# Optimization experiments

Hardware: AMD Instinct MI355X
Metric: run time of the kernel (lower is better)

The kernel has to match this reference:

```python
import jax, jax.numpy as jnp
import numpy as np

B, S, E = 8, 2048, 512
H = 8
LN_EPS = 1e-5


def _layer_norm(x, g, b):
    mu = jnp.mean(x, axis=-1, keepdims=True)
    var = jnp.mean((x - mu) ** 2, axis=-1, keepdims=True)
    return (x - mu) * jax.lax.rsqrt(var + LN_EPS) * g + b


def setup_inputs() -> dict:
    key = jax.random.key(0)
    ks = jax.random.split(key, 16)
    sc = 1.0 / np.sqrt(E)
    return {
        "q": jax.random.normal(ks[0], (B, S, E), jnp.float32),
        "k": jax.random.normal(ks[1], (B, S, E), jnp.float32),
        "trajectories": jax.random.normal(ks[2], (B, S, E), jnp.float32),
        "v_W": jax.random.normal(ks[3], (E, E), jnp.float32) * sc,
        "v_b": jnp.zeros((E,), jnp.float32),
        "out_W": jax.random.normal(ks[4], (E, E), jnp.float32) * sc,
        "out_b": jnp.zeros((E,), jnp.float32),
        "ln1_g": jnp.ones((E,), jnp.float32),
        "ln1_b": jnp.zeros((E,), jnp.float32),
        "ffn_w1": jax.random.normal(ks[5], (E, E), jnp.float32) * sc,
        "ffn_b1": jnp.zeros((E,), jnp.float32),
        "ffn_w2": jax.random.normal(ks[6], (E, E), jnp.float32) * sc,
        "ffn_b2": jnp.zeros((E,), jnp.float32),
        "ln2_g": jnp.ones((E,), jnp.float32),
        "ln2_b": jnp.zeros((E,), jnp.float32),
    }


def reference(q, k, trajectories, v_W, v_b, out_W, out_b, ln1_g, ln1_b,
              ffn_w1, ffn_b1, ffn_w2, ffn_b2, ln2_g, ln2_b):
    seq_len = q.shape[1]
    # V projection (v = k in the block's call). q_linear/k_linear are unused in the original forward.
    V = k @ v_W + v_b  # [B,S,E]; head split + per-head matmul + concat == single matmul

    # Multi-view trajectory similarity (TSMiniSimilarity), averaged over 4 views
    tn = trajectories / jnp.maximum(
        jnp.linalg.norm(trajectories, axis=-1, keepdims=True), 1e-12)
    c = jnp.einsum('bie,bje->bij', tn, tn)  # cosine similarity [B,S,S]
    aw = (jax.nn.sigmoid(c)
          + jax.nn.sigmoid(c * c)
          + jax.nn.sigmoid(jnp.exp(c - 1.0))
          + jax.nn.sigmoid(0.5 * c + 0.5)) * 0.25

    # First softmax over keys
    aw = jax.nn.softmax(aw, axis=-1)
    # ut_mask = triu(ones, diag=1); original fills where mask == 0 (lower triangle incl. diag)
    ut = jnp.triu(jnp.ones((seq_len, seq_len), dtype=bool), k=1)
    aw = jnp.where(ut, aw, -1e9)
    # Second softmax after masking
    aw = jax.nn.softmax(aw, axis=-1)

    attended = jnp.einsum('bij,bje->bie', aw, V)
    attn_out = attended @ out_W + out_b

    x = _layer_norm(q + attn_out, ln1_g, ln1_b)  # dropout is identity in eval
    h = jax.nn.relu(x @ ffn_w1 + ffn_b1) @ ffn_w2 + ffn_b2
    return _layer_norm(x + h, ln2_g, ln2_b)
```

## Files before the change

### kernel.cpp

```cpp
#include <hip/hip_runtime.h>

typedef __attribute__((ext_vector_type(8))) short s8v;
typedef __attribute__((ext_vector_type(4))) short s4v;
typedef __attribute__((ext_vector_type(4))) float f4v;

constexpr int SEQ = 2048;
constexpr int EMB = 512;
constexpr int BATCH = 8;
constexpr int BS = BATCH * SEQ;
constexpr int NCH = 32;

#define DEVINL __device__ __forceinline__

DEVINL float bf2f(short s) {
    union { unsigned u; float f; } v;
    v.u = ((unsigned)(unsigned short)s) << 16;
    return v.f;
}
DEVINL short f2bf(float f) {
    union { float f; unsigned u; } v; v.f = f;
    unsigned u = v.u;
    return (short)((u + 0x7FFFu + ((u >> 16) & 1u)) >> 16);
}
DEVINL f4v mfma16(s8v a, s8v b, f4v c) {
    return __builtin_amdgcn_mfma_f32_16x16x32_bf16(a, b, c, 0, 0, 0);
}
DEVINL s8v pack8(float4 a, float4 b) {
    s8v o;
    o[0] = f2bf(a.x); o[1] = f2bf(a.y); o[2] = f2bf(a.z); o[3] = f2bf(a.w);
    o[4] = f2bf(b.x); o[5] = f2bf(b.y); o[6] = f2bf(b.z); o[7] = f2bf(b.w);
    return o;
}
DEVINL void gload16(const short* g, short* l) {
    __builtin_amdgcn_global_load_lds(
        (const __attribute__((address_space(1))) void*)g,
        (__attribute__((address_space(3))) void*)l, 16, 0, 0);
}

__global__ __launch_bounds__(256) void prep_combo(
    const float* __restrict__ v_W, const float* __restrict__ out_W,
    const float* __restrict__ w1, const float* __restrict__ w2,
    const float* __restrict__ K, const float* __restrict__ v_b,
    const float* __restrict__ out_b,
    short* __restrict__ VWb, short* __restrict__ WoT,
    short* __restrict__ W1T, short* __restrict__ W2T,
    float* __restrict__ partial, float* __restrict__ bc) {
    __shared__ __attribute__((aligned(16))) char smem[4 * EMB * 4];
    const int blk = blockIdx.x;
    const int tid = threadIdx.x;

    if (blk < 128) {
        int i = blk * 256 + tid;
        const float* p = v_W + (size_t)i * 8;
        float4 a = *(const float4*)p;
        float4 b = *(const float4*)(p + 4);
        *(s8v*)(VWb + (size_t)i * 8) = pack8(a, b);
    } else if (blk < 320) {
        __shared__ short tile[64][72];
        int t = blk - 128;
        int sel = t >> 6;
        const float* W = (sel == 0) ? out_W : (sel == 1 ? w1 : w2);
        short* WT = (sel == 0) ? WoT : (sel == 1 ? W1T : W2T);
        int tileid = t & 63;
        int kt = (tileid >> 3) * 64, nt = (tileid & 7) * 64;
        int r = tid >> 4;
        int c4 = (tid & 15) * 4;
#pragma unroll
        for (int p = 0; p < 4; p++) {
            int row = p * 16 + r;
            float4 v = *(const float4*)(W + (size_t)(kt + row) * EMB + nt + c4);
            tile[row][c4 + 0] = f2bf(v.x);
            tile[row][c4 + 1] = f2bf(v.y);
            tile[row][c4 + 2] = f2bf(v.z);
            tile[row][c4 + 3] = f2bf(v.w);
        }
        __syncthreads();
        int kl = (tid & 7) * 8;
        int nl = tid >> 3;
#pragma unroll
        for (int h = 0; h < 2; h++) {
            int n = h * 32 + nl;
            s8v o;
#pragma unroll
            for (int e = 0; e < 8; e++) o[e] = tile[kl + e][n];
            *(s8v*)(WT + (size_t)(nt + n) * EMB + kt + kl) = o;
        }
    } else if (blk < 576) {
        float* sh = (float*)smem;
        int bb = blk - 320;
        int b = bb >> 5, c = bb & (NCH - 1);
        int g = tid >> 6, lane = tid & 63;
        int col8 = lane * 8;
        const float* base = K + ((size_t)b * SEQ + c * 64 + g * 16) * EMB + col8;
        float acc[8] = {};
        for (int it = 0; it < 16; it++) {
            float4 a = *(const float4*)(base + (size_t)it * EMB);
            float4 b2 = *(const float4*)(base + (size_t)it * EMB + 4);
            acc[0] += a.x; acc[1] += a.y; acc[2] += a.z; acc[3] += a.w;
            acc[4] += b2.x; acc[5] += b2.y; acc[6] += b2.z; acc[7] += b2.w;
        }
#pragma unroll
        for (int j = 0; j < 8; j++) sh[g * EMB + col8 + j] = acc[j];
        __syncthreads();
        if (g == 0) {
#pragma unroll
            for (int j = 0; j < 8; j++) {
                int e = col8 + j;
                partial[((size_t)b * NCH + c) * EMB + e] =
                    sh[e] + sh[EMB + e] + sh[2 * EMB + e] + sh[3 * EMB + e];
            }
        }
    } else {
        float* sh = (float*)smem;
        int bb = blk - 576;
        int nl = tid & 31, ms = tid >> 5;
        int n = bb * 32 + nl;
        float acc = 0.f;
#pragma unroll 8
        for (int mm = 0; mm < 64; mm++) {
            int m = ms * 64 + mm;
            acc = fmaf(v_b[m], out_W[(size_t)m * EMB + n], acc);
        }
        sh[tid] = acc;
        __syncthreads();
        if (tid < 32) {
            float s = 0.f;
#pragma unroll
            for (int j = 0; j < 8; j++) s += sh[j * 32 + tid];
            bc[bb * 32 + tid] = s + out_b[bb * 32 + tid];
        }
    }
}

template <int EPI>
__global__ __launch_bounds__(256, 2) void mgemm(
    const short* __restrict__ A, const short* __restrict__ B,
    const float* __restrict__ bias, short* __restrict__ C) {
    __shared__ __attribute__((aligned(16))) short lds[2][16384];

    const int nwg = gridDim.x;
    const int q = nwg >> 3;
    const int bid = blockIdx.x;
    const int wg = (bid & 7) * q + (bid >> 3);
    const int mt = wg >> 2, nt = wg & 3;
    const int mbase = mt * 128, nbase = nt * 128;

    const int tid = threadIdx.x;
    const int w = tid >> 6, lane = tid & 63;
    const int lr = lane & 15, kg = lane >> 4;
    const int wr = w >> 1, wc = w & 1;

    const short* gA[4];
    const short* gB[4];
    short* lA[4];
    short* lB[4];
#pragma unroll
    for (int inst = 0; inst < 4; inst++) {
        int U = inst * 256 + w * 64 + lane;
        int row = U >> 3, cu = U & 7;
        int csrc = cu ^ (row & 7);
        gA[inst] = A + (size_t)(mbase + row) * EMB + csrc * 8;
        gB[inst] = B + (size_t)(nbase + row) * EMB + csrc * 8;
        lA[inst] = &lds[0][(inst * 256 + w * 64) * 8];
        lB[inst] = &lds[0][8192 + (inst * 256 + w * 64) * 8];
    }

    int aoff[4][2], boff[4][2];
#pragma unroll
    for (int m = 0; m < 4; m++)
#pragma unroll
        for (int ks = 0; ks < 2; ks++) {
            int row = wr * 64 + m * 16 + lr;
            int cu = (ks * 4 + kg) ^ (row & 7);
            aoff[m][ks] = row * 64 + cu * 8;
        }
#pragma unroll
    for (int n = 0; n < 4; n++)
#pragma unroll
        for (int ks = 0; ks < 2; ks++) {
            int row = wc * 64 + n * 16 + lr;
            int cu = (ks * 4 + kg) ^ (row & 7);
            boff[n][ks] = 8192 + row * 64 + cu * 8;
        }

    auto stage = [&](int kt, int d) {
        int koff = kt * 64;
        int dd = d * 16384;
#pragma unroll
        for (int inst = 0; inst < 4; inst++)
            gload16(gA[inst] + koff, lA[inst] + dd);
#pragma unroll
        for (int inst = 0; inst < 4; inst++)
            gload16(gB[inst] + koff, lB[inst] + dd);
    };

    f4v acc[4][4] = {};
    stage(0, 0);
    int cur = 0;
    for (int kt = 0; kt < 8; kt++) {
        __syncthreads();
        if (kt < 7) stage(kt + 1, cur ^ 1);
        const short* base = &lds[cur][0];
        s8v afr[4][2], bfr[4][2];
#pragma unroll
        for (int m = 0; m < 4; m++)
#pragma unroll
            for (int ks = 0; ks < 2; ks++)
                afr[m][ks] = *(const s8v*)(base + aoff[m][ks]);
#pragma unroll
        for (int n = 0; n < 4; n++)
#pragma unroll
            for (int ks = 0; ks < 2; ks++)
                bfr[n][ks] = *(const s8v*)(base + boff[n][ks]);
#pragma unroll
        for (int ks = 0; ks < 2; ks++)
#pragma unroll
            for (int m = 0; m < 4; m++)
#pragma unroll
                for (int n = 0; n < 4; n++)
                    acc[m][n] = mfma16(afr[m][ks], bfr[n][ks], acc[m][n]);
        cur ^= 1;
    }

    if constexpr (EPI == 2) {
#pragma unroll
        for (int m = 0; m < 4; m++)
#pragma unroll
            for (int n = 0; n < 4; n++) {
                int col = nbase + wc * 64 + n * 16 + lr;
                int row0 = mbase + wr * 64 + m * 16 + kg * 4;
                s4v o;
#pragma unroll
                for (int r = 0; r < 4; r++) o[r] = f2bf(acc[m][n][r]);
                *(s4v*)(C + (size_t)col * EMB + row0) = o;
            }
    } else {
        float bcol[4];
#pragma unroll
        for (int n = 0; n < 4; n++)
            bcol[n] = bias[nbase + wc * 64 + n * 16 + lr];
#pragma unroll
        for (int m = 0; m < 4; m++)
#pragma unroll
            for (int n = 0; n < 4; n++) {
                int col = nbase + wc * 64 + n * 16 + lr;
#pragma unroll
                for (int r = 0; r < 4; r++) {
                    int row = mbase + wr * 64 + m * 16 + kg * 4 + r;
                    float v = acc[m][n][r] + bcol[n];
                    if constexpr (EPI == 1) v = fmaxf(v, 0.f);
                    C[(size_t)row * EMB + col] = f2bf(v);
                }
            }
    }
}

__global__ __launch_bounds__(256) void scan_p2(const float* __restrict__ K,
                                               const float* __restrict__ partial,
                                               short* __restrict__ SK) {
    __shared__ float wsum[4][EMB];
    int b = blockIdx.x >> 5, c = blockIdx.x & (NCH - 1);
    int g = threadIdx.x >> 6, lane = threadIdx.x & 63;
    int col8 = lane * 8;

    float off[8] = {}, alltot[8] = {};
    for (int cc = 0; cc < NCH; cc++) {
        const float* pp = partial + ((size_t)b * NCH + cc) * EMB + col8;
        float4 pa = *(const float4*)pp;
        float4 pb = *(const float4*)(pp + 4);
        float v[8] = {pa.x, pa.y, pa.z, pa.w, pb.x, pb.y, pb.z, pb.w};
#pragma unroll
        for (int j = 0; j < 8; j++) {
            alltot[j] += v[j];
            if (cc > c) off[j] += v[j];
        }
    }
    const float* base = K + ((size_t)b * SEQ + c * 64 + g * 16) * EMB + col8;
    {
        float acc[8] = {};
        for (int it = 0; it < 16; it++) {
            float4 a = *(const float4*)(base + (size_t)it * EMB);
            float4 bb = *(const float4*)(base + (size_t)it * EMB + 4);
            acc[0] += a.x; acc[1] += a.y; acc[2] += a.z; acc[3] += a.w;
            acc[4] += bb.x; acc[5] += bb.y; acc[6] += bb.z; acc[7] += bb.w;
        }
#pragma unroll
        for (int j = 0; j < 8; j++) wsum[g][col8 + j] = acc[j];
    }
    __syncthreads();
    float suf[8];
#pragma unroll
    for (int j = 0; j < 8; j++) {
        float s = off[j];
        for (int gg = g + 1; gg < 4; gg++) s += wsum[gg][col8 + j];
        suf[j] = s;
    }
    short* skbase = SK + ((size_t)b * SEQ + c * 64 + g * 16) * EMB + col8;
    for (int it = 15; it >= 0; it--) {
        int gi = c * 64 + g * 16 + it;
        float4 a = *(const float4*)(base + (size_t)it * EMB);
        float4 bb = *(const float4*)(base + (size_t)it * EMB + 4);
        s8v o;
        if (gi == SEQ - 1) {
            float inv = 1.0f / (float)SEQ;
#pragma unroll
            for (int j = 0; j < 8; j++) o[j] = f2bf(alltot[j] * inv);
        } else {
            float inv = __builtin_amdgcn_rcpf((float)(SEQ - 1 - gi));
#pragma unroll
            for (int j = 0; j < 8; j++) o[j] = f2bf(suf[j] * inv);
        }
        *(s8v*)(skbase + (size_t)it * EMB) = o;
        suf[0] += a.x; suf[1] += a.y; suf[2] += a.z; suf[3] += a.w;
        suf[4] += bb.x; suf[5] += bb.y; suf[6] += bb.z; suf[7] += bb.w;
    }
}

__global__ __launch_bounds__(256) void ln1_kernel(
    const float* __restrict__ q, const short* __restrict__ VO2,
    const float* __restrict__ gam, const float* __restrict__ bet,
    short* __restrict__ Xbf) {
    int w = threadIdx.x >> 6, lane = threadIdx.x & 63;
    int row0 = blockIdx.x * 32 + w * 8;
    for (int it = 0; it < 8; it++) {
        size_t grow = row0 + it;
        const float* qp = q + grow * EMB + lane * 8;
        float4 qa = *(const float4*)qp;
        float4 qb = *(const float4*)(qp + 4);
        s8v ao = *(const s8v*)(VO2 + grow * EMB + lane * 8);
        float v[8];
        v[0] = qa.x + bf2f(ao[0]); v[1] = qa.y + bf2f(ao[1]);
        v[2] = qa.z + bf2f(ao[2]); v[3] = qa.w + bf2f(ao[3]);
        v[4] = qb.x + bf2f(ao[4]); v[5] = qb.y + bf2f(ao[5]);
        v[6] = qb.z + bf2f(ao[6]); v[7] = qb.w + bf2f(ao[7]);
        float s = 0.f, t = 0.f;
#pragma unroll
        for (int j = 0; j < 8; j++) { s += v[j]; t += v[j] * v[j]; }
#pragma unroll
        for (int m = 32; m >= 1; m >>= 1) {
            s += __shfl_xor(s, m);
            t += __shfl_xor(t, m);
        }
        float mean = s * (1.f / EMB);
        float var = t * (1.f / EMB) - mean * mean;
        float rstd = rsqrtf(var + 1e-5f);
        s8v xb;
#pragma unroll
        for (int j = 0; j < 8; j++) {
            int col = lane * 8 + j;
            xb[j] = f2bf((v[j] - mean) * rstd * gam[col] + bet[col]);
        }
        *(s8v*)(Xbf + grow * EMB + lane * 8) = xb;
    }
}

__global__ __launch_bounds__(256) void ln2_kernel(
    const short* __restrict__ Xbf, const short* __restrict__ Y,
    const float* __restrict__ gam, const float* __restrict__ bet,
    float* __restrict__ out) {
    int w = threadIdx.x >> 6, lane = threadIdx.x & 63;
    int row0 = blockIdx.x * 32 + w * 8;
    for (int it = 0; it < 8; it++) {
        size_t grow = row0 + it;
        s8v xv = *(const s8v*)(Xbf + grow * EMB + lane * 8);
        s8v yv = *(const s8v*)(Y + grow * EMB + lane * 8);
        float v[8];
#pragma unroll
        for (int j = 0; j < 8; j++) v[j] = bf2f(xv[j]) + bf2f(yv[j]);
        float s = 0.f, t = 0.f;
#pragma unroll
        for (int j = 0; j < 8; j++) { s += v[j]; t += v[j] * v[j]; }
#pragma unroll
        for (int m = 32; m >= 1; m >>= 1) {
            s += __shfl_xor(s, m);
            t += __shfl_xor(t, m);
        }
        float mean = s * (1.f / EMB);
        float var = t * (1.f / EMB) - mean * mean;
        float rstd = rsqrtf(var + 1e-5f);
        float xo[8];
#pragma unroll
        for (int j = 0; j < 8; j++) {
            int col = lane * 8 + j;
            xo[j] = (v[j] - mean) * rstd * gam[col] + bet[col];
        }
        float* op = out + grow * EMB + lane * 8;
        *(float4*)op = make_float4(xo[0], xo[1], xo[2], xo[3]);
        *(float4*)(op + 4) = make_float4(xo[4], xo[5], xo[6], xo[7]);
    }
}


extern "C" void kernel_launch(void* const* d_in, const int* in_sizes, int n_in,
                              void* d_out, int out_size, void* d_ws, size_t ws_size,
                              hipStream_t stream) {
    (void)in_sizes; (void)n_in; (void)out_size; (void)ws_size;
    const float* q     = (const float*)d_in[0];
    const float* k     = (const float*)d_in[1];
    const float* v_W   = (const float*)d_in[3];
    const float* v_b   = (const float*)d_in[4];
    const float* out_W = (const float*)d_in[5];
    const float* out_b = (const float*)d_in[6];
    const float* ln1_g = (const float*)d_in[7];
    const float* ln1_b = (const float*)d_in[8];
    const float* w1    = (const float*)d_in[9];
    const float* b1    = (const float*)d_in[10];
    const float* w2    = (const float*)d_in[11];
    const float* b2    = (const float*)d_in[12];
    const float* ln2_g = (const float*)d_in[13];
    const float* ln2_b = (const float*)d_in[14];

    char* ws = (char*)d_ws;
    const size_t MB = 1u << 20;
    short* SK   = (short*)(ws);
    short* VO2  = (short*)(ws + 16 * MB);
    short* Xbf  = (short*)(ws + 32 * MB);
    short* H1   = (short*)(ws + 48 * MB);
    short* Y    = (short*)(ws + 64 * MB);
    short* VWb  = (short*)(ws + 80 * MB);
    short* WoT  = VWb + 512 * 512;
    short* W1T  = WoT + 512 * 512;
    short* W2T  = W1T + 512 * 512;
    short* WcT  = W2T + 512 * 512;
    float* bc   = (float*)(WcT + 512 * 512);
    float* part = bc + EMB;

    prep_combo<<<592, 256, 0, stream>>>(v_W, out_W, w1, w2, k, v_b, out_b,
                                        VWb, WoT, W1T, W2T, part, bc);
    mgemm<2><<<(EMB / 128) * 4, 256, 0, stream>>>(VWb, WoT, nullptr, WcT);
    scan_p2<<<BATCH * NCH, 256, 0, stream>>>(k, part, SK);
    mgemm<0><<<(BS / 128) * 4, 256, 0, stream>>>(SK, WcT, bc, VO2);
    ln1_kernel<<<BS / 32, 256, 0, stream>>>(q, VO2, ln1_g, ln1_b, Xbf);
    mgemm<1><<<(BS / 128) * 4, 256, 0, stream>>>(Xbf, W1T, b1, H1);
    mgemm<0><<<(BS / 128) * 4, 256, 0, stream>>>(H1, W2T, b2, Y);
    ln2_kernel<<<BS / 32, 256, 0, stream>>>(Xbf, Y, ln2_g, ln2_b, (float*)d_out);
}
```

Measured before the change: 104.3 us.

## Fuse all stages into one persistent kernel with grid-wide barriers

Replaces eight separate kernel launches with one persistent kernel of 512 blocks that runs every stage (weight prep, scan, four GEMMs, two layernorms) and separates them with a software grid barrier built on atomics. The aim is to remove launch overhead and the idle tails between dependent kernels. It relies on all 512 blocks being co-resident (two per CU with 64KB LDS each), otherwise the barrier deadlocks. Each barrier is a serialising point with atomic spinning, and the shared 64KB LDS buffer may lower occupancy for the non-GEMM phases.

```diff
diff --git a/kernel.cpp b/kernel.cpp
--- a/kernel.cpp
+++ b/kernel.cpp
@@ -9,6 +9,7 @@
 constexpr int BATCH = 8;
 constexpr int BS = BATCH * SEQ;
 constexpr int NCH = 32;
+constexpr int NBLK = 512;
 
 #define DEVINL __device__ __forceinline__
 
@@ -37,27 +38,42 @@
         (__attribute__((address_space(3))) void*)l, 16, 0, 0);
 }
 
-__global__ __launch_bounds__(256) void prep_combo(
-    const float* __restrict__ v_W, const float* __restrict__ out_W,
-    const float* __restrict__ w1, const float* __restrict__ w2,
-    const float* __restrict__ K, const float* __restrict__ v_b,
-    const float* __restrict__ out_b,
-    short* __restrict__ VWb, short* __restrict__ WoT,
-    short* __restrict__ W1T, short* __restrict__ W2T,
-    float* __restrict__ partial, float* __restrict__ bc) {
-    __shared__ __attribute__((aligned(16))) char smem[4 * EMB * 4];
-    const int blk = blockIdx.x;
-    const int tid = threadIdx.x;
-
-    if (blk < 128) {
-        int i = blk * 256 + tid;
+DEVINL void gridbar(unsigned* cnt, unsigned* gen) {
+    __syncthreads();
+    if (threadIdx.x == 0) {
+        unsigned g = __hip_atomic_load(gen, __ATOMIC_RELAXED,
+                                       __HIP_MEMORY_SCOPE_AGENT);
+        unsigned a = __hip_atomic_fetch_add(cnt, 1u, __ATOMIC_ACQ_REL,
+                                            __HIP_MEMORY_SCOPE_AGENT);
+        if (a == (unsigned)(NBLK - 1)) {
+            __hip_atomic_store(cnt, 0u, __ATOMIC_RELAXED,
+                               __HIP_MEMORY_SCOPE_AGENT);
+            __hip_atomic_store(gen, g + 1u, __ATOMIC_RELEASE,
+                               __HIP_MEMORY_SCOPE_AGENT);
+        } else {
+            while (__hip_atomic_load(gen, __ATOMIC_ACQUIRE,
+                                     __HIP_MEMORY_SCOPE_AGENT) == g)
+                __builtin_amdgcn_s_sleep(2);
+        }
+    }
+    __syncthreads();
+}
+
+
+DEVINL void prep_item(int item, int tid, char* Ub,
+                      const float* v_W, const float* out_W, const float* w1,
+                      const float* w2, const float* K, const float* v_b,
+                      const float* out_b, short* VWb, short* WoT, short* W1T,
+                      short* W2T, float* partial, float* bc) {
+    if (item < 128) {
+        int i = item * 256 + tid;
         const float* p = v_W + (size_t)i * 8;
         float4 a = *(const float4*)p;
         float4 b = *(const float4*)(p + 4);
         *(s8v*)(VWb + (size_t)i * 8) = pack8(a, b);
-    } else if (blk < 320) {
-        __shared__ short tile[64][72];
-        int t = blk - 128;
+    } else if (item < 320) {
+        short(*tile)[72] = (short(*)[72])Ub;
+        int t = item - 128;
         int sel = t >> 6;
         const float* W = (sel == 0) ? out_W : (sel == 1 ? w1 : w2);
         short* WT = (sel == 0) ? WoT : (sel == 1 ? W1T : W2T);
@@ -85,9 +101,9 @@
             for (int e = 0; e < 8; e++) o[e] = tile[kl + e][n];
             *(s8v*)(WT + (size_t)(nt + n) * EMB + kt + kl) = o;
         }
-    } else if (blk < 576) {
-        float* sh = (float*)smem;
-        int bb = blk - 320;
+    } else if (item < 576) {
+        float* sh = (float*)Ub;
+        int bb = item - 320;
         int b = bb >> 5, c = bb & (NCH - 1);
         int g = tid >> 6, lane = tid & 63;
         int col8 = lane * 8;
@@ -111,8 +127,8 @@
             }
         }
     } else {
-        float* sh = (float*)smem;
-        int bb = blk - 576;
+        float* sh = (float*)Ub;
+        int bb = item - 576;
         int nl = tid & 31, ms = tid >> 5;
         int n = bb * 32 + nl;
         float acc = 0.f;
@@ -132,135 +148,11 @@
     }
 }
 
-template <int EPI>
-__global__ __launch_bounds__(256, 2) void mgemm(
-    const short* __restrict__ A, const short* __restrict__ B,
-    const float* __restrict__ bias, short* __restrict__ C) {
-    __shared__ __attribute__((aligned(16))) short lds[2][16384];
-
-    const int nwg = gridDim.x;
-    const int q = nwg >> 3;
-    const int bid = blockIdx.x;
-    const int wg = (bid & 7) * q + (bid >> 3);
-    const int mt = wg >> 2, nt = wg & 3;
-    const int mbase = mt * 128, nbase = nt * 128;
-
-    const int tid = threadIdx.x;
-    const int w = tid >> 6, lane = tid & 63;
-    const int lr = lane & 15, kg = lane >> 4;
-    const int wr = w >> 1, wc = w & 1;
-
-    const short* gA[4];
-    const short* gB[4];
-    short* lA[4];
-    short* lB[4];
-#pragma unroll
-    for (int inst = 0; inst < 4; inst++) {
-        int U = inst * 256 + w * 64 + lane;
-        int row = U >> 3, cu = U & 7;
-        int csrc = cu ^ (row & 7);
-        gA[inst] = A + (size_t)(mbase + row) * EMB + csrc * 8;
-        gB[inst] = B + (size_t)(nbase + row) * EMB + csrc * 8;
-        lA[inst] = &lds[0][(inst * 256 + w * 64) * 8];
-        lB[inst] = &lds[0][8192 + (inst * 256 + w * 64) * 8];
-    }
-
-    int aoff[4][2], boff[4][2];
-#pragma unroll
-    for (int m = 0; m < 4; m++)
-#pragma unroll
-        for (int ks = 0; ks < 2; ks++) {
-            int row = wr * 64 + m * 16 + lr;
-            int cu = (ks * 4 + kg) ^ (row & 7);
-            aoff[m][ks] = row * 64 + cu * 8;
-        }
-#pragma unroll
-    for (int n = 0; n < 4; n++)
-#pragma unroll
-        for (int ks = 0; ks < 2; ks++) {
-            int row = wc * 64 + n * 16 + lr;
-            int cu = (ks * 4 + kg) ^ (row & 7);
-            boff[n][ks] = 8192 + row * 64 + cu * 8;
-        }
-
-    auto stage = [&](int kt, int d) {
-        int koff = kt * 64;
-        int dd = d * 16384;
-#pragma unroll
-        for (int inst = 0; inst < 4; inst++)
-            gload16(gA[inst] + koff, lA[inst] + dd);
-#pragma unroll
-        for (int inst = 0; inst < 4; inst++)
-            gload16(gB[inst] + koff, lB[inst] + dd);
-    };
-
-    f4v acc[4][4] = {};
-    stage(0, 0);
-    int cur = 0;
-    for (int kt = 0; kt < 8; kt++) {
-        __syncthreads();
-        if (kt < 7) stage(kt + 1, cur ^ 1);
-        const short* base = &lds[cur][0];
-        s8v afr[4][2], bfr[4][2];
-#pragma unroll
-        for (int m = 0; m < 4; m++)
-#pragma unroll
-            for (int ks = 0; ks < 2; ks++)
-                afr[m][ks] = *(const s8v*)(base + aoff[m][ks]);
-#pragma unroll
-        for (int n = 0; n < 4; n++)
-#pragma unroll
-            for (int ks = 0; ks < 2; ks++)
-                bfr[n][ks] = *(const s8v*)(base + boff[n][ks]);
-#pragma unroll
-        for (int ks = 0; ks < 2; ks++)
-#pragma unroll
-            for (int m = 0; m < 4; m++)
-#pragma unroll
-                for (int n = 0; n < 4; n++)
-                    acc[m][n] = mfma16(afr[m][ks], bfr[n][ks], acc[m][n]);
-        cur ^= 1;
-    }
-
-    if constexpr (EPI == 2) {
-#pragma unroll
-        for (int m = 0; m < 4; m++)
-#pragma unroll
-            for (int n = 0; n < 4; n++) {
-                int col = nbase + wc * 64 + n * 16 + lr;
-                int row0 = mbase + wr * 64 + m * 16 + kg * 4;
-                s4v o;
-#pragma unroll
-                for (int r = 0; r < 4; r++) o[r] = f2bf(acc[m][n][r]);
-                *(s4v*)(C + (size_t)col * EMB + row0) = o;
-            }
-    } else {
-        float bcol[4];
-#pragma unroll
-        for (int n = 0; n < 4; n++)
-            bcol[n] = bias[nbase + wc * 64 + n * 16 + lr];
-#pragma unroll
-        for (int m = 0; m < 4; m++)
-#pragma unroll
-            for (int n = 0; n < 4; n++) {
-                int col = nbase + wc * 64 + n * 16 + lr;
-#pragma unroll
-                for (int r = 0; r < 4; r++) {
-                    int row = mbase + wr * 64 + m * 16 + kg * 4 + r;
-                    float v = acc[m][n][r] + bcol[n];
-                    if constexpr (EPI == 1) v = fmaxf(v, 0.f);
-                    C[(size_t)row * EMB + col] = f2bf(v);
-                }
-            }
-    }
-}
-
-__global__ __launch_bounds__(256) void scan_p2(const float* __restrict__ K,
-                                               const float* __restrict__ partial,
-                                               short* __restrict__ SK) {
-    __shared__ float wsum[4][EMB];
-    int b = blockIdx.x >> 5, c = blockIdx.x & (NCH - 1);
-    int g = threadIdx.x >> 6, lane = threadIdx.x & 63;
+DEVINL void scan2_item(int bid, int tid, char* Ub, const float* K,
+                       const float* partial, short* SK) {
+    float* wsum = (float*)Ub;
+    int b = bid >> 5, c = bid & (NCH - 1);
+    int g = tid >> 6, lane = tid & 63;
     int col8 = lane * 8;
 
     float off[8] = {}, alltot[8] = {};
@@ -285,14 +177,14 @@
             acc[4] += bb.x; acc[5] += bb.y; acc[6] += bb.z; acc[7] += bb.w;
         }
 #pragma unroll
-        for (int j = 0; j < 8; j++) wsum[g][col8 + j] = acc[j];
+        for (int j = 0; j < 8; j++) wsum[g * EMB + col8 + j] = acc[j];
     }
     __syncthreads();
     float suf[8];
 #pragma unroll
     for (int j = 0; j < 8; j++) {
         float s = off[j];
-        for (int gg = g + 1; gg < 4; gg++) s += wsum[gg][col8 + j];
+        for (int gg = g + 1; gg < 4; gg++) s += wsum[gg * EMB + col8 + j];
         suf[j] = s;
     }
     short* skbase = SK + ((size_t)b * SEQ + c * 64 + g * 16) * EMB + col8;
@@ -316,12 +208,126 @@
     }
 }
 
-__global__ __launch_bounds__(256) void ln1_kernel(
-    const float* __restrict__ q, const short* __restrict__ VO2,
-    const float* __restrict__ gam, const float* __restrict__ bet,
-    short* __restrict__ Xbf) {
-    int w = threadIdx.x >> 6, lane = threadIdx.x & 63;
-    int row0 = blockIdx.x * 32 + w * 8;
+template <int EPI>
+DEVINL void gemm_tile(char* Ub, int wg, int tid, const short* A,
+                      const short* B, const float* bias, short* C) {
+    short* L = (short*)Ub;
+    const int mt = wg >> 2, nt = wg & 3;
+    const int mbase = mt * 128, nbase = nt * 128;
+    const int w = tid >> 6, lane = tid & 63;
+    const int lr = lane & 15, kg = lane >> 4;
+    const int wr = w >> 1, wc = w & 1;
+
+    const short* gA[4];
+    const short* gB[4];
+    short* lA[4];
+    short* lB[4];
+#pragma unroll
+    for (int inst = 0; inst < 4; inst++) {
+        int Ui = inst * 256 + w * 64 + lane;
+        int row = Ui >> 3, cu = Ui & 7;
+        int csrc = cu ^ (row & 7);
+        gA[inst] = A + (size_t)(mbase + row) * EMB + csrc * 8;
+        gB[inst] = B + (size_t)(nbase + row) * EMB + csrc * 8;
+        lA[inst] = L + (inst * 256 + w * 64) * 8;
+        lB[inst] = L + 8192 + (inst * 256 + w * 64) * 8;
+    }
+
+    int aoff[4][2], boff[4][2];
+#pragma unroll
+    for (int m = 0; m < 4; m++)
+#pragma unroll
+        for (int ks = 0; ks < 2; ks++) {
+            int row = wr * 64 + m * 16 + lr;
+            int cu = (ks * 4 + kg) ^ (row & 7);
+            aoff[m][ks] = row * 64 + cu * 8;
+        }
+#pragma unroll
+    for (int n = 0; n < 4; n++)
+#pragma unroll
+        for (int ks = 0; ks < 2; ks++) {
+            int row = wc * 64 + n * 16 + lr;
+            int cu = (ks * 4 + kg) ^ (row & 7);
+            boff[n][ks] = 8192 + row * 64 + cu * 8;
+        }
+
+    auto stage = [&](int kt, int d) {
+        int koff = kt * 64;
+        int dd = d * 16384;
+#pragma unroll
+        for (int inst = 0; inst < 4; inst++)
+            gload16(gA[inst] + koff, lA[inst] + dd);
+#pragma unroll
+        for (int inst = 0; inst < 4; inst++)
+            gload16(gB[inst] + koff, lB[inst] + dd);
+    };
+
+    f4v acc[4][4] = {};
+    stage(0, 0);
+    int cur = 0;
+    for (int kt = 0; kt < 8; kt++) {
+        __syncthreads();
+        if (kt < 7) stage(kt + 1, cur ^ 1);
+        const short* base = L + cur * 16384;
+        s8v afr[4][2], bfr[4][2];
+#pragma unroll
+        for (int m = 0; m < 4; m++)
+#pragma unroll
+            for (int ks = 0; ks < 2; ks++)
+                afr[m][ks] = *(const s8v*)(base + aoff[m][ks]);
+#pragma unroll
+        for (int n = 0; n < 4; n++)
+#pragma unroll
+            for (int ks = 0; ks < 2; ks++)
+                bfr[n][ks] = *(const s8v*)(base + boff[n][ks]);
+#pragma unroll
+        for (int ks = 0; ks < 2; ks++)
+#pragma unroll
+            for (int m = 0; m < 4; m++)
+#pragma unroll
+                for (int n = 0; n < 4; n++)
+                    acc[m][n] = mfma16(afr[m][ks], bfr[n][ks], acc[m][n]);
+        cur ^= 1;
+    }
+    __syncthreads();
+
+    if constexpr (EPI == 2) {
+#pragma unroll
+        for (int m = 0; m < 4; m++)
+#pragma unroll
+            for (int n = 0; n < 4; n++) {
+                int col = nbase + wc * 64 + n * 16 + lr;
+                int row0 = mbase + wr * 64 + m * 16 + kg * 4;
+                s4v o;
+#pragma unroll
+                for (int r = 0; r < 4; r++) o[r] = f2bf(acc[m][n][r]);
+                *(s4v*)(C + (size_t)col * EMB + row0) = o;
+            }
+    } else {
+        float bcol[4];
+#pragma unroll
+        for (int n = 0; n < 4; n++)
+            bcol[n] = bias[nbase + wc * 64 + n * 16 + lr];
+#pragma unroll
+        for (int m = 0; m < 4; m++)
+#pragma unroll
+            for (int n = 0; n < 4; n++) {
+                int col = nbase + wc * 64 + n * 16 + lr;
+#pragma unroll
+                for (int r = 0; r < 4; r++) {
+                    int row = mbase + wr * 64 + m * 16 + kg * 4 + r;
+                    float v = acc[m][n][r] + bcol[n];
+                    if constexpr (EPI == 1) v = fmaxf(v, 0.f);
+                    C[(size_t)row * EMB + col] = f2bf(v);
+                }
+            }
+    }
+}
+
+DEVINL void ln1_body(int bid, int tid, const float* q, const short* VO2,
+                     const float* gam, const float* bet, short* Xbf) {
+    int w = tid >> 6, lane = tid & 63;
+    int row0 = bid * 32 + w * 8;
     for (int it = 0; it < 8; it++) {
         size_t grow = row0 + it;
         const float* qp = q + grow * EMB + lane * 8;
@@ -354,12 +360,10 @@
     }
 }
 
-__global__ __launch_bounds__(256) void ln2_kernel(
-    const short* __restrict__ Xbf, const short* __restrict__ Y,
-    const float* __restrict__ gam, const float* __restrict__ bet,
-    float* __restrict__ out) {
-    int w = threadIdx.x >> 6, lane = threadIdx.x & 63;
-    int row0 = blockIdx.x * 32 + w * 8;
+DEVINL void ln2_body(int bid, int tid, const short* Xbf, const short* Y,
+                     const float* gam, const float* bet, float* out) {
+    int w = tid >> 6, lane = tid & 63;
+    int row0 = bid * 32 + w * 8;
     for (int it = 0; it < 8; it++) {
         size_t grow = row0 + it;
         s8v xv = *(const s8v*)(Xbf + grow * EMB + lane * 8);
@@ -388,6 +392,50 @@
         *(float4*)op = make_float4(xo[0], xo[1], xo[2], xo[3]);
         *(float4*)(op + 4) = make_float4(xo[4], xo[5], xo[6], xo[7]);
     }
+}
+
+__global__ __launch_bounds__(256, 2) void mega(
+    const float* __restrict__ q, const float* __restrict__ K,
+    const float* __restrict__ v_W, const float* __restrict__ v_b,
+    const float* __restrict__ out_W, const float* __restrict__ out_b,
+    const float* __restrict__ ln1_g, const float* __restrict__ ln1_b,
+    const float* __restrict__ w1, const float* __restrict__ b1,
+    const float* __restrict__ w2, const float* __restrict__ b2,
+    const float* __restrict__ ln2_g, const float* __restrict__ ln2_b,
+    short* VWb, short* WoT, short* W1T, short* W2T, short* WcT,
+    float* bc, float* part, short* SK, short* VO2, short* Xbf, short* H1,
+    short* Y, float* out, unsigned* cnt, unsigned* gen) {
+    __shared__ __attribute__((aligned(16))) char Ub[65536];
+    const int bid = blockIdx.x;
+    const int tid = threadIdx.x;
+
+    for (int item = bid; item < 592; item += NBLK) {
+        prep_item(item, tid, Ub, v_W, out_W, w1, w2, K, v_b, out_b,
+                  VWb, WoT, W1T, W2T, part, bc);
+        __syncthreads();
+    }
+    gridbar(cnt, gen);
+
+    if (bid < 16)
+        gemm_tile<2>(Ub, (bid & 7) * 2 + (bid >> 3), tid, VWb, WoT, nullptr,
+                     WcT);
+    else if (bid < 272)
+        scan2_item(bid - 16, tid, Ub, K, part, SK);
+    gridbar(cnt, gen);
+
+    gemm_tile<0>(Ub, (bid & 7) * 64 + (bid >> 3), tid, SK, WcT, bc, VO2);
+    gridbar(cnt, gen);
+
+    ln1_body(bid, tid, q, VO2, ln1_g, ln1_b, Xbf);
+    gridbar(cnt, gen);
+
+    gemm_tile<1>(Ub, (bid & 7) * 64 + (bid >> 3), tid, Xbf, W1T, b1, H1);
+    gridbar(cnt, gen);
+
+    gemm_tile<0>(Ub, (bid & 7) * 64 + (bid >> 3), tid, H1, W2T, b2, Y);
+    gridbar(cnt, gen);
+
+    ln2_body(bid, tid, Xbf, Y, ln2_g, ln2_b, out);
 }
 
 
@@ -424,14 +472,12 @@
     short* WcT  = W2T + 512 * 512;
     float* bc   = (float*)(WcT + 512 * 512);
     float* part = bc + EMB;
-
-    prep_combo<<<592, 256, 0, stream>>>(v_W, out_W, w1, w2, k, v_b, out_b,
-                                        VWb, WoT, W1T, W2T, part, bc);
-    mgemm<2><<<(EMB / 128) * 4, 256, 0, stream>>>(VWb, WoT, nullptr, WcT);
-    scan_p2<<<BATCH * NCH, 256, 0, stream>>>(k, part, SK);
-    mgemm<0><<<(BS / 128) * 4, 256, 0, stream>>>(SK, WcT, bc, VO2);
-    ln1_kernel<<<BS / 32, 256, 0, stream>>>(q, VO2, ln1_g, ln1_b, Xbf);
-    mgemm<1><<<(BS / 128) * 4, 256, 0, stream>>>(Xbf, W1T, b1, H1);
-    mgemm<0><<<(BS / 128) * 4, 256, 0, stream>>>(H1, W2T, b2, Y);
-    ln2_kernel<<<BS / 32, 256, 0, stream>>>(Xbf, Y, ln2_g, ln2_b, (float*)d_out);
-}
+    unsigned* bar = (unsigned*)(ws + 88 * MB);
+
+    hipMemsetAsync(bar, 0, 256, stream);
+    mega<<<NBLK, 256, 0, stream>>>(q, k, v_W, v_b, out_W, out_b, ln1_g, ln1_b,
+                                   w1, b1, w2, b2, ln2_g, ln2_b,
+                                   VWb, WoT, W1T, W2T, WcT, bc, part,
+                                   SK, VO2, Xbf, H1, Y, (float*)d_out, bar,
+                                   bar + 64);
+}
```

New measurement: 379.5 us. 3.64x slower.
